# Performance work log

Hardware: AMD Instinct MI355X
Metric: run time of the kernel (lower is better)

The kernel has to match this reference:

```python
import jax, jax.numpy as jnp
import numpy as np

B, N, D = 16, 1024, 1024  # head_count = 1, N must equal D for shapes to close


def setup_inputs() -> dict:
    key = jax.random.key(0)
    kx, kk, kq, kv, kr = jax.random.split(key, 5)
    s = 1.0 / np.sqrt(D)  # keep pre-softmax logits in a sane range
    return {
        "x": jax.random.normal(kx, (B, N, D), dtype=jnp.float32),
        "Wk": jax.random.normal(kk, (D, D), dtype=jnp.float32) * s,
        "Wq": jax.random.normal(kq, (D, D), dtype=jnp.float32) * s,
        "Wv": jax.random.normal(kv, (D, D), dtype=jnp.float32) * s,
        "Wr": jax.random.normal(kr, (D, D), dtype=jnp.float32) * s,
    }


def reference(x, Wk, Wq, Wv, Wr):
    # torch nn.Linear(bias=False): y = x @ W.T
    keys = x @ Wk.T      # [B, N, D]
    queries = x @ Wq.T   # [B, N, D]
    values = x @ Wv.T    # [B, N, D]

    d = Wk.shape[0]  # head_key_channels = head_value_channels = D (head_count=1)
    # Faithful to the torch code: slice dim=1 (tokens) to the first D entries.
    # With N == D this is the full tensor.
    key = jax.nn.softmax(keys[:, :d, :], axis=2)      # softmax over channels
    query = jax.nn.softmax(queries[:, :d, :], axis=1)  # softmax over tokens
    value = values[:, :d, :]

    # context = key @ value^T : [B, d, d]
    context = jnp.einsum('bnd,bmd->bnm', key, value)
    # attended = context^T @ query : [B, d, D]
    attended = jnp.einsum('bnm,bnd->bmd', context, query)

    return attended @ Wr.T  # [B, d, D]
```

## Files before the change

### kernel.cpp

```cpp
#include <hip/hip_runtime.h>

typedef unsigned short u16;
typedef unsigned int u32;
typedef __attribute__((ext_vector_type(4))) float f32x4;
typedef __attribute__((ext_vector_type(8))) short bf16x8;
typedef __attribute__((ext_vector_type(4))) u16 u16x4;
typedef __attribute__((ext_vector_type(8))) u16 u16x8;

#define B_ 16
#define N_ 1024
#define D_ 1024
#define BM 256
#define BN 256
#define BK 64

__device__ __forceinline__ float bf2f(u16 v) {
  return __uint_as_float((u32)v << 16);
}
__device__ __forceinline__ u16 f2bf(float f) {
  u32 u = __float_as_uint(f);
  return (u16)((u + 0x7FFFu + ((u >> 16) & 1u)) >> 16);
}
__device__ __forceinline__ void gload_lds16(const void* g, void* l) {
  __builtin_amdgcn_global_load_lds(
      (const __attribute__((address_space(1))) void*)g,
      (__attribute__((address_space(3))) void*)l, 16, 0, 0);
}

__global__ __launch_bounds__(256) void cast_kernel(const float* __restrict__ in,
                                                   u16* __restrict__ out, int n4) {
  const int stride = gridDim.x * blockDim.x;
  for (int i = blockIdx.x * blockDim.x + threadIdx.x; i < n4; i += stride) {
    float4 v = ((const float4*)in)[i];
    u16x4 o;
    o[0] = f2bf(v.x); o[1] = f2bf(v.y); o[2] = f2bf(v.z); o[3] = f2bf(v.w);
    ((u16x4*)out)[i] = o;
  }
}

__global__ __launch_bounds__(256) void cast4_kernel(
    const float* __restrict__ w0, const float* __restrict__ w1,
    const float* __restrict__ w2, const float* __restrict__ w3,
    u16* __restrict__ out) {
  const int per = (D_ * D_) / 4;
  const int stride = gridDim.x * blockDim.x;
  for (int i = blockIdx.x * blockDim.x + threadIdx.x; i < 4 * per; i += stride) {
    const int w = i / per, r = i - w * per;
    const float* src = (w == 0) ? w0 : (w == 1) ? w1 : (w == 2) ? w2 : w3;
    float4 v = ((const float4*)src)[r];
    u16x4 o;
    o[0] = f2bf(v.x); o[1] = f2bf(v.y); o[2] = f2bf(v.z); o[3] = f2bf(v.w);
    ((u16x4*)out)[i] = o;
  }
}

template <typename OutT, bool SPLITC>
__global__ __launch_bounds__(512, 2) void gemm_bt256(
    const u16* __restrict__ A, const u16* __restrict__ Bm, OutT* __restrict__ C,
    long long sA, long long sB, long long sC, int tx_n, int nb_per) {
  __shared__ u16 lds[4][2][128 * 64];
  const int tid = threadIdx.x;
  const int lane = tid & 63;
  const int wid = tid >> 6;
  const int wm = wid >> 2;
  const int wn = wid & 3;
  const int rl = lane & 15, kl = lane >> 4;

  const int nwg = gridDim.x;
  const int orig = blockIdx.x;
  const int wgid = (orig & 7) * (nwg >> 3) + (orig >> 3);
  const int batch = wgid / nb_per;
  const int rem = wgid % nb_per;
  const int row0 = (rem / tx_n) * BM;
  const int col0 = (rem % tx_n) * BN;
  A += (long long)batch * sA;
  Bm += (long long)batch * sB;
  OutT* Cb;
  if constexpr (SPLITC) {
    Cb = C + (size_t)(col0 >> 10) * ((size_t)16384 * 1024) + (col0 & 1023);
  } else {
    Cb = C + (long long)batch * sC + col0;
  }

  const char* lb = (const char*)&lds[0][0][0];
  char* lw = (char*)&lds[0][0][0];

  const u32 swz = (u32)((kl * 16) ^ ((rl & 7) << 4));
  const u32 vA0 = (u32)(wm * 32768 + rl * 128) + swz;
  const u32 vA1 = vA0 ^ 64u;
  const u32 vB0 = (u32)((2 + (wn >> 1)) * 32768 + (wn & 1) * 8192 + rl * 128) + swz;
  const u32 vB1 = vB0 ^ 64u;
#define RDA(BUF, MI, KK) \
  (*(const bf16x8*)(lb + ((KK) ? vA1 : vA0) + ((BUF) * 16384 + (MI) * 2048)))
#define RDB(BUF, NI, KK) \
  (*(const bf16x8*)(lb + ((KK) ? vB1 : vB0) + ((BUF) * 16384 + (NI) * 2048)))

  const int r0 = tid >> 3;
  const u32 li0 = (u32)(((tid & 7) * 16) ^ ((r0 & 7) << 4));
  const u16* gA0 = A + (size_t)(row0 + r0) * 1024 + (li0 >> 1);
  const u16* gB0 = Bm + (size_t)(col0 + r0) * 1024 + (li0 >> 1);
#define STAGE_A(H, BUF, T)                                                    \
  do {                                                                        \
    gload_lds16(gA0 + (size_t)((H)*128 + 0) * 1024 + (T)*64,                  \
                lw + (H)*32768 + (BUF)*16384 + tid * 16);                     \
    gload_lds16(gA0 + (size_t)((H)*128 + 64) * 1024 + (T)*64,                 \
                lw + (H)*32768 + (BUF)*16384 + 8192 + tid * 16);              \
  } while (0)
#define STAGE_B(H, BUF, T)                                                    \
  do {                                                                        \
    gload_lds16(gB0 + (size_t)((H)*128 + 0) * 1024 + (T)*64,                  \
                lw + (2 + (H)) * 32768 + (BUF)*16384 + tid * 16);             \
    gload_lds16(gB0 + (size_t)((H)*128 + 64) * 1024 + (T)*64,                 \
                lw + (2 + (H)) * 32768 + (BUF)*16384 + 8192 + tid * 16);      \
  } while (0)

  f32x4 acc[8][4] = {};
  bf16x8 aF[4][2], bF[2][2], bG[2][2];

  auto mfma16 = [&](int rb, int cb, bf16x8 (&bb)[2][2]) {
#pragma unroll
    for (int kk = 0; kk < 2; ++kk)
#pragma unroll
      for (int mi = 0; mi < 4; ++mi)
#pragma unroll
        for (int ni = 0; ni < 2; ++ni)
          acc[rb + mi][cb + ni] = __builtin_amdgcn_mfma_f32_16x16x32_bf16(
              aF[mi][kk], bb[ni][kk], acc[rb + mi][cb + ni], 0, 0, 0);
  };

#define SBAR() __builtin_amdgcn_sched_barrier(0)
#define BAR() __builtin_amdgcn_s_barrier()
#define TILE(T, BUF, OBUF, STHA, STHB, GATE)                                  \
  {                                                                           \
                         \
    _Pragma("unroll") for (int mi = 0; mi < 4; ++mi) {                        \
      aF[mi][0] = RDA(BUF, mi, 0); aF[mi][1] = RDA(BUF, mi, 1);               \
    }                                                                         \
    _Pragma("unroll") for (int ni = 0; ni < 2; ++ni) {                        \
      bF[ni][0] = RDB(BUF, ni, 0); bF[ni][1] = RDB(BUF, ni, 1);               \
    }                                                                         \
    if (STHA) STAGE_A(0, OBUF, (T) + 1);                                      \
    asm volatile("s_waitcnt lgkmcnt(8)" ::: "memory");                        \
    SBAR(); BAR();                                                            \
    __builtin_amdgcn_s_setprio(1);                                            \
    mfma16(0, 0, bF);                                                         \
    __builtin_amdgcn_s_setprio(0);                                            \
    SBAR(); BAR();                                                            \
                                      \
    _Pragma("unroll") for (int ni = 0; ni < 2; ++ni) {                        \
      bG[ni][0] = RDB(BUF, 2 + ni, 0); bG[ni][1] = RDB(BUF, 2 + ni, 1);       \
    }                                                                         \
    if (STHA) STAGE_A(1, OBUF, (T) + 1);                                      \
    SBAR(); BAR();                                                            \
    __builtin_amdgcn_s_setprio(1);                                            \
    mfma16(0, 2, bG);                                                         \
    __builtin_amdgcn_s_setprio(0);                                            \
    SBAR(); BAR();                                                            \
        \
    _Pragma("unroll") for (int mi = 0; mi < 4; ++mi) {                        \
      aF[mi][0] = RDA(BUF, 4 + mi, 0); aF[mi][1] = RDA(BUF, 4 + mi, 1);       \
    }                                                                         \
    if (STHB) STAGE_B(0, BUF, (T) + 2);                                       \
    SBAR(); BAR();                                                            \
    __builtin_amdgcn_s_setprio(1);                                            \
    mfma16(4, 2, bG);                                                         \
    __builtin_amdgcn_s_setprio(0);                                            \
    SBAR(); BAR();                                                            \
                                  \
    if (STHB) STAGE_B(1, BUF, (T) + 2);                                       \
    __builtin_amdgcn_s_setprio(1);                                            \
    mfma16(4, 0, bF);                                                         \
    __builtin_amdgcn_s_setprio(0);                                            \
    SBAR();                                                                   \
    if ((GATE) == 0) asm volatile("s_waitcnt vmcnt(4)" ::: "memory");         \
    else if ((GATE) == 1) asm volatile("s_waitcnt vmcnt(0)" ::: "memory");    \
    if ((GATE) != 2) BAR();                                                   \
  }

  STAGE_A(0, 0, 0); STAGE_A(1, 0, 0);
  STAGE_B(0, 0, 0); STAGE_B(1, 0, 0);
  STAGE_B(0, 1, 1); STAGE_B(1, 1, 1);
  asm volatile("s_waitcnt vmcnt(4)" ::: "memory");
  BAR();

#pragma unroll 1
  for (int u = 0; u < 7; ++u) {
    const int T0 = 2 * u;
    TILE(T0, 0, 1, 1, 1, 0);
    TILE(T0 + 1, 1, 0, 1, 1, 0);
  }
  TILE(14, 0, 1, 1, 0, 1);
  TILE(15, 1, 0, 0, 0, 2);

#undef TILE
#undef SBAR
#undef BAR
#undef RDA
#undef RDB
#undef STAGE_A
#undef STAGE_B

#pragma unroll
  for (int mi = 0; mi < 8; ++mi)
#pragma unroll
    for (int ni = 0; ni < 4; ++ni)
#pragma unroll
      for (int j = 0; j < 4; ++j) {
        const int rr = row0 + wm * 128 + mi * 16 + kl * 4 + j;
        const int cc = wn * 64 + ni * 16 + rl;
        const float v = acc[mi][ni][j];
        if constexpr (sizeof(OutT) == 2)
          Cb[(size_t)rr * 1024 + cc] = (OutT)f2bf(v);
        else
          Cb[(size_t)rr * 1024 + cc] = v;
      }
}

__global__ __launch_bounds__(256) void key_sm_t(const u16* __restrict__ Kp,
                                                u16* __restrict__ KT) {
  const int b = blockIdx.y, n0 = blockIdx.x * 64;
  const int tid = threadIdx.x, lane = tid & 63, w = tid >> 6;
  __shared__ float smax[64], sinv[64];
  __shared__ u16 Tl[64][72];
  const u16* base = Kp + ((size_t)b * N_ + n0) * D_;
  for (int i = 0; i < 16; ++i) {
    const int r = w * 16 + i;
    const u16x8* rp = (const u16x8*)(base + (size_t)r * D_ + lane * 16);
    u16x8 v0 = rp[0], v1 = rp[1];
    float f[16];
#pragma unroll
    for (int j = 0; j < 8; ++j) { f[j] = bf2f(v0[j]); f[8 + j] = bf2f(v1[j]); }
    float m = -1e30f;
#pragma unroll
    for (int j = 0; j < 16; ++j) m = fmaxf(m, f[j]);
    for (int off = 32; off; off >>= 1) m = fmaxf(m, __shfl_xor(m, off));
    float s = 0.f;
#pragma unroll
    for (int j = 0; j < 16; ++j) s += __expf(f[j] - m);
    for (int off = 32; off; off >>= 1) s += __shfl_xor(s, off);
    if (lane == 0) { smax[r] = m; sinv[r] = 1.f / s; }
  }
  __syncthreads();
  for (int ct = 0; ct < 16; ++ct) {
    const int r = tid >> 2, cb = (tid & 3) * 16;
    const u16x8* rp = (const u16x8*)(base + (size_t)r * D_ + ct * 64 + cb);
    u16x8 v0 = rp[0], v1 = rp[1];
    const float m = smax[r], inv = sinv[r];
#pragma unroll
    for (int j = 0; j < 8; ++j) {
      Tl[r][cb + j] = f2bf(__expf(bf2f(v0[j]) - m) * inv);
      Tl[r][cb + 8 + j] = f2bf(__expf(bf2f(v1[j]) - m) * inv);
    }
    __syncthreads();
    const int c = tid >> 2, nb = (tid & 3) * 16;
    u16x8 o0, o1;
#pragma unroll
    for (int e = 0; e < 8; ++e) { o0[e] = Tl[nb + e][c]; o1[e] = Tl[nb + 8 + e][c]; }
    u16x8* op = (u16x8*)(KT + ((size_t)b * D_ + ct * 64 + c) * N_ + n0 + nb);
    op[0] = o0; op[1] = o1;
    __syncthreads();
  }
}

__global__ __launch_bounds__(256) void query_sm_t(const u16* __restrict__ Qp,
                                                  u16* __restrict__ QT) {
  const int b = blockIdx.y, d0 = blockIdx.x * 64;
  const int tid = threadIdx.x, l = tid & 63, g = tid >> 6;
  __shared__ float pm[4][64], ps[4][64];
  __shared__ float cmax[64], cinv[64];
  __shared__ u16 Tl[64][72];
  const u16* base = Qp + (size_t)b * N_ * D_;
  float m = -1e30f, s = 0.f;
  for (int n = g * 256; n < g * 256 + 256; ++n) {
    const float x = bf2f(base[(size_t)n * D_ + d0 + l]);
    const float nm = fmaxf(m, x);
    s = s * __expf(m - nm) + __expf(x - nm);
    m = nm;
  }
  pm[g][l] = m; ps[g][l] = s;
  __syncthreads();
  if (tid < 64) {
    float M = pm[0][tid];
    for (int k2 = 1; k2 < 4; ++k2) M = fmaxf(M, pm[k2][tid]);
    float S = 0.f;
    for (int k2 = 0; k2 < 4; ++k2) S += ps[k2][tid] * __expf(pm[k2][tid] - M);
    cmax[tid] = M; cinv[tid] = 1.f / S;
  }
  __syncthreads();
  for (int nt = 0; nt < 16; ++nt) {
    const int r = tid >> 2, cb = (tid & 3) * 16;
    const u16x8* rp = (const u16x8*)(base + (size_t)(nt * 64 + r) * D_ + d0 + cb);
    u16x8 v0 = rp[0], v1 = rp[1];
#pragma unroll
    for (int j = 0; j < 8; ++j) {
      Tl[r][cb + j] = f2bf(__expf(bf2f(v0[j]) - cmax[cb + j]) * cinv[cb + j]);
      Tl[r][cb + 8 + j] =
          f2bf(__expf(bf2f(v1[j]) - cmax[cb + 8 + j]) * cinv[cb + 8 + j]);
    }
    __syncthreads();
    const int c = tid >> 2, nb = (tid & 3) * 16;
    u16x8 o0, o1;
#pragma unroll
    for (int e = 0; e < 8; ++e) { o0[e] = Tl[nb + e][c]; o1[e] = Tl[nb + 8 + e][c]; }
    u16x8* op = (u16x8*)(QT + ((size_t)b * D_ + d0 + c) * N_ + nt * 64 + nb);
    op[0] = o0; op[1] = o1;
    __syncthreads();
  }
}

extern "C" void kernel_launch(void* const* d_in, const int* in_sizes, int n_in,
                              void* d_out, int out_size, void* d_ws, size_t ws_size,
                              hipStream_t stream) {
  const float* x = (const float*)d_in[0];
  const float* Wk = (const float*)d_in[1];
  const float* Wq = (const float*)d_in[2];
  const float* Wv = (const float*)d_in[3];
  const float* Wr = (const float*)d_in[4];
  float* out = (float*)d_out;
  char* ws = (char*)d_ws;
  const size_t MB = 1ull << 20;

  u16* Xb  = (u16*)(ws + 0 * MB);
  u16* KT  = (u16*)(ws + 0 * MB);
  u16* Wkb = (u16*)(ws + 32 * MB);
  u16* Wrb = (u16*)(ws + 38 * MB);
  u16* Kp  = (u16*)(ws + 40 * MB);
  u16* St  = (u16*)(ws + 40 * MB);
  u16* Qp  = (u16*)(ws + 72 * MB);
  u16* Att = (u16*)(ws + 72 * MB);
  u16* V   = (u16*)(ws + 104 * MB);
  u16* QT  = (u16*)(ws + 136 * MB);

  const int nX = B_ * N_ * D_;
  cast_kernel<<<2048, 256, 0, stream>>>(x, Xb, nX / 4);
  cast4_kernel<<<1024, 256, 0, stream>>>(Wk, Wq, Wv, Wr, Wkb);

  gemm_bt256<u16, true><<<768, 512, 0, stream>>>(Xb, Wkb, Kp, 0, 0, 0, 12, 768);

  key_sm_t<<<dim3(N_ / 64, B_), 256, 0, stream>>>(Kp, KT);
  query_sm_t<<<dim3(D_ / 64, B_), 256, 0, stream>>>(Qp, QT);

  const long long sNN = (long long)N_ * D_;
  gemm_bt256<u16, false><<<256, 512, 0, stream>>>(QT, KT, St, sNN, sNN, sNN, 4, 16);
  gemm_bt256<u16, false><<<256, 512, 0, stream>>>(V, St, Att, sNN, sNN, sNN, 4, 16);
  gemm_bt256<float, false><<<256, 512, 0, stream>>>(Att, Wrb, out, 0, 0, 0, 4, 256);
}
```

Baseline: 295.9 us.

## Restructure GEMM tile barriers and move last MFMA block after the vmcnt gate

Cuts the per-tile barriers from seven to four. Each LDS fragment read is now followed by an explicit lgkmcnt(0) wait plus barrier, and the final MFMA block is moved after the global-load wait and barrier so it overlaps with the next tile's start. LDS read and write pointers are precomputed per thread to cut address arithmetic. The cost is a full lgkmcnt(0) wait instead of the partial lgkmcnt(8), and the moved MFMAs could shift the race window between buffer reuse and the async loads.

```diff
diff --git a/kernel.cpp b/kernel.cpp
--- a/kernel.cpp
+++ b/kernel.cpp
@@ -83,17 +83,21 @@
   }
 
   const char* lb = (const char*)&lds[0][0][0];
-  char* lw = (char*)&lds[0][0][0];
-
-  const u32 swz = (u32)((kl * 16) ^ ((rl & 7) << 4));
-  const u32 vA0 = (u32)(wm * 32768 + rl * 128) + swz;
-  const u32 vA1 = vA0 ^ 64u;
-  const u32 vB0 = (u32)((2 + (wn >> 1)) * 32768 + (wn & 1) * 8192 + rl * 128) + swz;
-  const u32 vB1 = vB0 ^ 64u;
+  char* lwt = (char*)&lds[0][0][0] + tid * 16;
+
+  const u32 mask = (u32)((rl & 7) << 4);
+  const u32 cs0 = ((u32)(kl * 16)) ^ mask;
+  const u32 cs1 = ((u32)(64 + kl * 16)) ^ mask;
+  const char* pAk0 = lb + wm * 32768 + rl * 128 + cs0;
+  const char* pAk1 = lb + wm * 32768 + rl * 128 + cs1;
+  const char* pBk0 =
+      lb + (2 + (wn >> 1)) * 32768 + (wn & 1) * 8192 + rl * 128 + cs0;
+  const char* pBk1 =
+      lb + (2 + (wn >> 1)) * 32768 + (wn & 1) * 8192 + rl * 128 + cs1;
 #define RDA(BUF, MI, KK) \
-  (*(const bf16x8*)(lb + ((KK) ? vA1 : vA0) + ((BUF) * 16384 + (MI) * 2048)))
+  (*(const bf16x8*)(((KK) ? pAk1 : pAk0) + (BUF)*16384 + (MI)*2048))
 #define RDB(BUF, NI, KK) \
-  (*(const bf16x8*)(lb + ((KK) ? vB1 : vB0) + ((BUF) * 16384 + (NI) * 2048)))
+  (*(const bf16x8*)(((KK) ? pBk1 : pBk0) + (BUF)*16384 + (NI)*2048))
 
   const int r0 = tid >> 3;
   const u32 li0 = (u32)(((tid & 7) * 16) ^ ((r0 & 7) << 4));
@@ -102,16 +106,16 @@
 #define STAGE_A(H, BUF, T)                                                    \
   do {                                                                        \
     gload_lds16(gA0 + (size_t)((H)*128 + 0) * 1024 + (T)*64,                  \
-                lw + (H)*32768 + (BUF)*16384 + tid * 16);                     \
+                lwt + (H)*32768 + (BUF)*16384);                               \
     gload_lds16(gA0 + (size_t)((H)*128 + 64) * 1024 + (T)*64,                 \
-                lw + (H)*32768 + (BUF)*16384 + 8192 + tid * 16);              \
+                lwt + (H)*32768 + (BUF)*16384 + 8192);                        \
   } while (0)
 #define STAGE_B(H, BUF, T)                                                    \
   do {                                                                        \
     gload_lds16(gB0 + (size_t)((H)*128 + 0) * 1024 + (T)*64,                  \
-                lw + (2 + (H)) * 32768 + (BUF)*16384 + tid * 16);             \
+                lwt + (2 + (H)) * 32768 + (BUF)*16384);                       \
     gload_lds16(gB0 + (size_t)((H)*128 + 64) * 1024 + (T)*64,                 \
-                lw + (2 + (H)) * 32768 + (BUF)*16384 + 8192 + tid * 16);      \
+                lwt + (2 + (H)) * 32768 + (BUF)*16384 + 8192);                \
   } while (0)
 
   f32x4 acc[8][4] = {};
@@ -130,9 +134,10 @@
 
 #define SBAR() __builtin_amdgcn_sched_barrier(0)
 #define BAR() __builtin_amdgcn_s_barrier()
+#define LGKM0() asm volatile("s_waitcnt lgkmcnt(0)" ::: "memory")
 #define TILE(T, BUF, OBUF, STHA, STHB, GATE)                                  \
   {                                                                           \
-                         \
+           \
     _Pragma("unroll") for (int mi = 0; mi < 4; ++mi) {                        \
       aF[mi][0] = RDA(BUF, mi, 0); aF[mi][1] = RDA(BUF, mi, 1);               \
     }                                                                         \
@@ -140,41 +145,39 @@
       bF[ni][0] = RDB(BUF, ni, 0); bF[ni][1] = RDB(BUF, ni, 1);               \
     }                                                                         \
     if (STHA) STAGE_A(0, OBUF, (T) + 1);                                      \
-    asm volatile("s_waitcnt lgkmcnt(8)" ::: "memory");                        \
-    SBAR(); BAR();                                                            \
+    LGKM0(); SBAR(); BAR(); SBAR();                                           \
     __builtin_amdgcn_s_setprio(1);                                            \
     mfma16(0, 0, bF);                                                         \
     __builtin_amdgcn_s_setprio(0);                                            \
-    SBAR(); BAR();                                                            \
-                                      \
+                       \
     _Pragma("unroll") for (int ni = 0; ni < 2; ++ni) {                        \
       bG[ni][0] = RDB(BUF, 2 + ni, 0); bG[ni][1] = RDB(BUF, 2 + ni, 1);       \
     }                                                                         \
     if (STHA) STAGE_A(1, OBUF, (T) + 1);                                      \
-    SBAR(); BAR();                                                            \
+    LGKM0(); SBAR(); BAR(); SBAR();                                           \
     __builtin_amdgcn_s_setprio(1);                                            \
     mfma16(0, 2, bG);                                                         \
     __builtin_amdgcn_s_setprio(0);                                            \
-    SBAR(); BAR();                                                            \
-        \
+          \
     _Pragma("unroll") for (int mi = 0; mi < 4; ++mi) {                        \
       aF[mi][0] = RDA(BUF, 4 + mi, 0); aF[mi][1] = RDA(BUF, 4 + mi, 1);       \
     }                                                                         \
+    LGKM0(); SBAR(); BAR(); SBAR();                                           \
     if (STHB) STAGE_B(0, BUF, (T) + 2);                                       \
-    SBAR(); BAR();                                                            \
+    SBAR();                                                                   \
     __builtin_amdgcn_s_setprio(1);                                            \
     mfma16(4, 2, bG);                                                         \
     __builtin_amdgcn_s_setprio(0);                                            \
-    SBAR(); BAR();                                                            \
-                                  \
+                         \
     if (STHB) STAGE_B(1, BUF, (T) + 2);                                       \
-    __builtin_amdgcn_s_setprio(1);                                            \
-    mfma16(4, 0, bF);                                                         \
-    __builtin_amdgcn_s_setprio(0);                                            \
     SBAR();                                                                   \
     if ((GATE) == 0) asm volatile("s_waitcnt vmcnt(4)" ::: "memory");         \
     else if ((GATE) == 1) asm volatile("s_waitcnt vmcnt(0)" ::: "memory");    \
     if ((GATE) != 2) BAR();                                                   \
+    SBAR();                                                                   \
+    __builtin_amdgcn_s_setprio(1);                                            \
+    mfma16(4, 0, bF);                                                         \
+    __builtin_amdgcn_s_setprio(0);                                            \
   }
 
   STAGE_A(0, 0, 0); STAGE_A(1, 0, 0);
@@ -185,9 +188,8 @@
 
 #pragma unroll 1
   for (int u = 0; u < 7; ++u) {
-    const int T0 = 2 * u;
-    TILE(T0, 0, 1, 1, 1, 0);
-    TILE(T0 + 1, 1, 0, 1, 1, 0);
+    TILE(2 * u, 0, 1, 1, 1, 0);
+    TILE(2 * u + 1, 1, 0, 1, 1, 0);
   }
   TILE(14, 0, 1, 1, 0, 1);
   TILE(15, 1, 0, 0, 0, 2);
@@ -195,6 +197,7 @@
 #undef TILE
 #undef SBAR
 #undef BAR
+#undef LGKM0
 #undef RDA
 #undef RDB
 #undef STAGE_A
```

New measurement: 294.7 us. No clear change (-0.4%).
